# Kernel tuning notes

Hardware: AMD Instinct MI355X
Metric: run time of the kernel (lower is better)

Reference implementation:

```python
import jax, jax.numpy as jnp
import numpy as np

B, S, D, H, OUT = 256, 256, 512, 512, 128  # batch, time points, state dim (= hidden_size), MLP hidden, out_features


def setup_inputs() -> dict:
    key = jax.random.key(0)
    ks = jax.random.split(key, 6)
    # time channel: shared monotone grid (forward uses t[0] as the integration grid)
    t = jnp.linspace(0.0, 1.0, S)
    feats = jax.random.normal(ks[0], (B, S, D), dtype=jnp.float32) * 0.1
    x = jnp.concatenate([jnp.broadcast_to(t[None, :, None], (B, S, 1)), feats], axis=-1)  # [B,S,D+1]
    s1 = 1.0 / np.sqrt(D).astype(np.float32)
    s2 = 1.0 / np.sqrt(H).astype(np.float32)
    W1 = jax.random.normal(ks[1], (H, D), dtype=jnp.float32) * s1
    b1 = jnp.zeros((H,), dtype=jnp.float32)
    W2 = jax.random.normal(ks[2], (D, H), dtype=jnp.float32) * s2
    b2 = jnp.zeros((D,), dtype=jnp.float32)
    Wout = jax.random.normal(ks[3], (OUT, H), dtype=jnp.float32) * s2
    bout = jnp.zeros((OUT,), dtype=jnp.float32)
    return dict(x=x, W1=W1, b1=b1, W2=W2, b2=b2, Wout=Wout, bout=bout)


def reference(x, W1, b1, W2, b2, Wout, bout):
    t = x[0, :, 0]          # [S] integration grid (first sample's time channel)
    y0 = x[:, -1, 1:]       # [B, D] initial state

    def f(y):               # ODEFunc MLP: d -> h -> d
        return jnp.tanh(y @ W1.T + b1) @ W2.T + b2

    dts = t[1:] - t[:-1]    # [S-1]

    def rk4_step(y, dt):
        k1 = f(y)
        k2 = f(y + 0.5 * dt * k1)
        k3 = f(y + 0.5 * dt * k2)
        k4 = f(y + dt * k3)
        y_next = y + (dt / 6.0) * (k1 + 2.0 * k2 + 2.0 * k3 + k4)
        return y_next, None

    yT, _ = jax.lax.scan(rk4_step, y0, dts)  # solution[-1]: [B, D]
    return yT @ Wout.T + bout                # [B, OUT]
```

## Files before the change

kernel.cpp:

```cpp
#include <hip/hip_runtime.h>
#include <hip/hip_bf16.h>

typedef __attribute__((ext_vector_type(8))) short short8;
typedef __attribute__((ext_vector_type(8))) unsigned short ushort8;
typedef __attribute__((ext_vector_type(4))) float f32x4;
typedef __attribute__((ext_vector_type(4))) int int4v;
typedef __attribute__((ext_vector_type(4))) short short4v;

#define NB 256
#define NS 256
#define NH 512
#define NOUT 128
#define XROW 513

#define NCL 16
#define RPC 16
#define BPC 4
#define UBS 128
#define LPAD 520

#define OFF_DTS   0
#define OFF_Y0    4096
#define OFF_U0    (OFF_Y0 + NB*NH*4)
#define OFF_M     (OFF_U0 + NB*NH*4)
#define OFF_C     (OFF_M + NH*NH*2)
#define OFF_P     (OFF_C + 4096)
#define OFF_HG    (OFF_P + NOUT*NH*4)
#define OFF_HACC  (OFF_HG + NCL*2*RPC*NH*2)
#define OFF_FLAGS (OFF_HACC + NB*NH*4)

static __device__ __forceinline__ unsigned short bf16bits(float x) {
  return __builtin_bit_cast(unsigned short, __float2bfloat16(x));
}

static __device__ __forceinline__ void g_store8(void* addr, short4v v) {
  asm volatile("global_store_dwordx2 %0, %1, off sc0 sc1" :: "v"(addr), "v"(v) : "memory");
}
static __device__ __forceinline__ void g_store4(void* addr, unsigned v) {
  asm volatile("global_store_dword %0, %1, off sc0 sc1" :: "v"(addr), "v"(v) : "memory");
}
static __device__ __forceinline__ unsigned g_load4w(const void* addr) {
  unsigned v;
  asm volatile("global_load_dword %0, %1, off sc0 sc1\n\ts_waitcnt vmcnt(0)"
               : "=v"(v) : "v"(addr) : "memory");
  return v;
}
static __device__ __forceinline__ int4v g_load16(const void* addr) {
  int4v v;
  asm volatile("global_load_dwordx4 %0, %1, off sc0 sc1" : "=v"(v) : "v"(addr) : "memory");
  return v;
}
static __device__ __forceinline__ void wait_vm0() {
  asm volatile("s_waitcnt vmcnt(0)" ::: "memory");
}

static __device__ __forceinline__ float tanh_fast(float x) {
  x = fminf(fmaxf(x, -15.f), 15.f);
  float e = __expf(2.f * x);
  return (e - 1.f) * __builtin_amdgcn_rcpf(e + 1.f);
}


__global__ void k_dts(const float* __restrict__ x, float* __restrict__ dts) {
  int s = threadIdx.x;
  if (s < NS - 1) dts[s] = x[(s + 1) * XROW] - x[s * XROW];
  if (s == NS - 1) dts[NS - 1] = x[(NS - 1) * XROW] - x[0];
}

__global__ void k_y0(const float* __restrict__ x, float* __restrict__ y0) {
  int b = blockIdx.x;
  const float* src = x + (size_t)b * NS * XROW + (size_t)(NS - 1) * XROW + 1;
  for (int d = threadIdx.x; d < NH; d += blockDim.x) y0[b * NH + d] = src[d];
}

__global__ void k_c(const float* __restrict__ W1, const float* __restrict__ b2,
                    float* __restrict__ c) {
  int i = blockIdx.x * blockDim.x + threadIdx.x;
  if (i < NH) {
    float s = 0.f;
    for (int d = 0; d < NH; ++d) s += W1[i * NH + d] * b2[d];
    c[i] = s;
  }
}

__global__ void k_mm_nn_bf16(const float* __restrict__ A, const float* __restrict__ Bm,
                             __hip_bfloat16* __restrict__ C, int N, int K) {
  __shared__ float As[16][17], Bs[16][17];
  int tx = threadIdx.x & 15, ty = threadIdx.x >> 4;
  int m = blockIdx.y * 16 + ty, n = blockIdx.x * 16 + tx;
  float acc = 0.f;
  for (int k0 = 0; k0 < K; k0 += 16) {
    As[ty][tx] = A[m * K + k0 + tx];
    Bs[ty][tx] = Bm[(size_t)(k0 + ty) * N + n];
    __syncthreads();
#pragma unroll
    for (int kk = 0; kk < 16; ++kk) acc += As[ty][kk] * Bs[kk][tx];
    __syncthreads();
  }
  C[m * N + n] = __float2bfloat16(acc);
}

__global__ void k_mm_nn_f32(const float* __restrict__ A, const float* __restrict__ Bm,
                            float* __restrict__ C, int N, int K) {
  __shared__ float As[16][17], Bs[16][17];
  int tx = threadIdx.x & 15, ty = threadIdx.x >> 4;
  int m = blockIdx.y * 16 + ty, n = blockIdx.x * 16 + tx;
  float acc = 0.f;
  for (int k0 = 0; k0 < K; k0 += 16) {
    As[ty][tx] = A[m * K + k0 + tx];
    Bs[ty][tx] = Bm[(size_t)(k0 + ty) * N + n];
    __syncthreads();
#pragma unroll
    for (int kk = 0; kk < 16; ++kk) acc += As[ty][kk] * Bs[kk][tx];
    __syncthreads();
  }
  C[m * N + n] = acc;
}

__global__ void k_mm_nt_f32(const float* __restrict__ A, const float* __restrict__ Bm,
                            float* __restrict__ C, int N, int K) {
  __shared__ float As[16][17], Bs[16][17];
  int tx = threadIdx.x & 15, ty = threadIdx.x >> 4;
  int m = blockIdx.y * 16 + ty;
  int n0 = blockIdx.x * 16;
  float acc = 0.f;
  for (int k0 = 0; k0 < K; k0 += 16) {
    As[ty][tx] = A[m * K + k0 + tx];
    Bs[ty][tx] = Bm[(size_t)(n0 + ty) * K + k0 + tx];
    __syncthreads();
#pragma unroll
    for (int kk = 0; kk < 16; ++kk) acc += As[ty][kk] * Bs[tx][kk];
    __syncthreads();
  }
  C[m * N + n0 + tx] = acc;
}


__global__ __launch_bounds__(256) void k_main(
    const float* __restrict__ u0, const __hip_bfloat16* __restrict__ Mg,
    const float* __restrict__ cg, const float* __restrict__ b1g,
    const float* __restrict__ dtsg,
    __hip_bfloat16* __restrict__ hG, float* __restrict__ Hacc,
    unsigned int* __restrict__ flags)
{
  __shared__ __hip_bfloat16 Mlds[UBS][LPAD];
  __shared__ __hip_bfloat16 hlds[RPC][LPAD];
  __shared__ float dtl[NS];

  const int tid = threadIdx.x;
  const int bx = blockIdx.x;
  const int xcd = bx & 7, slot = bx >> 3;
  const int cl = xcd + ((slot >> 2) << 3);
  const int jb = slot & 3;
  const int lane = tid & 63, wv = tid >> 6;
  const int r = lane & 15, g4 = lane >> 4;
  const int row0 = cl * RPC;
  const int ub = jb * UBS;

  for (int i = tid; i < UBS * 64; i += 256) {
    int row = i >> 6, ch = (i & 63) * 8;
    *(ushort8*)&Mlds[row][ch] = *(const ushort8*)(Mg + (size_t)(ub + row) * NH + ch);
  }
  if (tid < NS) dtl[tid] = dtsg[tid];

  const int udl0 = wv * 32 + g4 * 4;
  float u[2][4], Wa[2][4], Hs[2][4], Ht[2][4], hr[2][4], wp[2][4];
  float b1r[2][4], cr[2][4];
#pragma unroll
  for (int t = 0; t < 2; ++t)
#pragma unroll
    for (int j = 0; j < 4; ++j) {
      int ud = ub + udl0 + t * 16 + j;
      u[t][j] = u0[(row0 + r) * NH + ud];
      b1r[t][j] = b1g[ud];
      cr[t][j] = cg[ud];
      Ht[t][j] = 0.f; wp[t][j] = 0.f; Wa[t][j] = 0.f; Hs[t][j] = 0.f;
    }
  __syncthreads();

  unsigned int* flg = flags + cl * 32;

  int sidx = 0;
  for (int step = 0; step < NS - 1; ++step) {
    float dt = dtl[step];
#pragma unroll 1
    for (int st = 0; st < 4; ++st, ++sidx) {
      float gam = (st == 0) ? 0.f : ((st == 3) ? dt : 0.5f * dt);
#pragma unroll
      for (int t = 0; t < 2; ++t)
#pragma unroll
        for (int j = 0; j < 4; ++j)
          hr[t][j] = tanh_fast(u[t][j] + gam * wp[t][j] + b1r[t][j]);

      int par = sidx & 1;
      __hip_bfloat16* hgp = hG + (size_t)(cl * 2 + par) * RPC * NH;
#pragma unroll
      for (int t = 0; t < 2; ++t) {
        short4v pk;
        pk.x = (short)bf16bits(hr[t][0]);
        pk.y = (short)bf16bits(hr[t][1]);
        pk.z = (short)bf16bits(hr[t][2]);
        pk.w = (short)bf16bits(hr[t][3]);
        int col = ub + udl0 + t * 16;
        g_store8(hgp + r * NH + col, pk);
        *(short4v*)&hlds[r][col] = pk;
      }
      wait_vm0();
      unsigned tgt = (unsigned)(sidx + 1);
      if (lane == 0) g_store4(flg + jb * 4 + wv, tgt);
      __syncthreads();

      f32x4 acc0 = {0.f, 0.f, 0.f, 0.f}, acc1 = {0.f, 0.f, 0.f, 0.f};
#pragma unroll
      for (int q = 0; q < 4; ++q) {
        int kc = ub + q * 32 + g4 * 8;
        short8 bf = *(const short8*)&hlds[r][kc];
        short8 a0 = *(const short8*)&Mlds[wv * 32 + r][kc];
        short8 a1 = *(const short8*)&Mlds[wv * 32 + 16 + r][kc];
        acc0 = __builtin_amdgcn_mfma_f32_16x16x32_bf16(a0, bf, acc0, 0, 0, 0);
        acc1 = __builtin_amdgcn_mfma_f32_16x16x32_bf16(a1, bf, acc1, 0, 0, 0);
      }

      {
        const unsigned int* fp = flg + (lane & 15);
        for (;;) {
          unsigned v = g_load4w(fp);
          if (__all((int)(v >= tgt))) break;
          __builtin_amdgcn_s_sleep(1);
        }
      }

      {
        int rr = tid >> 4, sl = tid & 15;
        int4v dv[3];
#pragma unroll
        for (int m = 0; m < 3; ++m) {
          int jr = (jb + 1 + m) & 3;
          dv[m] = g_load16(hgp + rr * NH + jr * UBS + sl * 8);
        }
        wait_vm0();
#pragma unroll
        for (int m = 0; m < 3; ++m) {
          int jr = (jb + 1 + m) & 3;
          *(int4v*)&hlds[rr][jr * UBS + sl * 8] = dv[m];
        }
      }
      __syncthreads();

#pragma unroll 1
      for (int m = 0; m < 3; ++m) {
        int jr = (jb + 1 + m) & 3;
#pragma unroll
        for (int q = 0; q < 4; ++q) {
          int kc = jr * UBS + q * 32 + g4 * 8;
          short8 bf = *(const short8*)&hlds[r][kc];
          short8 a0 = *(const short8*)&Mlds[wv * 32 + r][kc];
          short8 a1 = *(const short8*)&Mlds[wv * 32 + 16 + r][kc];
          acc0 = __builtin_amdgcn_mfma_f32_16x16x32_bf16(a0, bf, acc0, 0, 0, 0);
          acc1 = __builtin_amdgcn_mfma_f32_16x16x32_bf16(a1, bf, acc1, 0, 0, 0);
        }
      }

      float wc[2][4];
#pragma unroll
      for (int j = 0; j < 4; ++j) { wc[0][j] = acc0[j] + cr[0][j]; wc[1][j] = acc1[j] + cr[1][j]; }

      float cw = (st == 0 || st == 3) ? 1.f : 2.f;
#pragma unroll
      for (int t = 0; t < 2; ++t)
#pragma unroll
        for (int j = 0; j < 4; ++j) {
          if (st == 0) { Wa[t][j] = wc[t][j]; Hs[t][j] = hr[t][j]; }
          else { Wa[t][j] += cw * wc[t][j]; Hs[t][j] += cw * hr[t][j]; }
          wp[t][j] = wc[t][j];
        }
      if (st == 3) {
        float f6 = dt * (1.f / 6.f);
#pragma unroll
        for (int t = 0; t < 2; ++t)
#pragma unroll
          for (int j = 0; j < 4; ++j) {
            u[t][j] += f6 * Wa[t][j];
            Ht[t][j] += f6 * Hs[t][j];
          }
      }
    }
  }

#pragma unroll
  for (int t = 0; t < 2; ++t)
#pragma unroll
    for (int j = 0; j < 4; ++j)
      Hacc[(row0 + r) * NH + ub + udl0 + t * 16 + j] = Ht[t][j];
}

__global__ void k_epi(const float* __restrict__ y0, const float* __restrict__ Hacc,
                      const float* __restrict__ P, const float* __restrict__ Wout,
                      const float* __restrict__ b2, const float* __restrict__ bout,
                      const float* __restrict__ dtsg, float* __restrict__ out)
{
  __shared__ float ys[NH], hs[NH];
  int rr = blockIdx.x, o = threadIdx.x;
  float sdt = dtsg[NS - 1];
  for (int i = threadIdx.x; i < NH; i += blockDim.x) {
    ys[i] = y0[rr * NH + i] + sdt * b2[i];
    hs[i] = Hacc[rr * NH + i];
  }
  __syncthreads();
  float s = bout[o];
  const float* wr = Wout + o * NH;
  const float* pr = P + o * NH;
  for (int d = 0; d < NH; ++d) s += wr[d] * ys[d];
  for (int h = 0; h < NH; ++h) s += pr[h] * hs[h];
  out[rr * NOUT + o] = s;
}


extern "C" void kernel_launch(void* const* d_in, const int* in_sizes, int n_in,
                              void* d_out, int out_size, void* d_ws, size_t ws_size,
                              hipStream_t stream) {
  const float* x    = (const float*)d_in[0];
  const float* W1   = (const float*)d_in[1];
  const float* b1   = (const float*)d_in[2];
  const float* W2   = (const float*)d_in[3];
  const float* b2   = (const float*)d_in[4];
  const float* Wout = (const float*)d_in[5];
  const float* bout = (const float*)d_in[6];
  float* out = (float*)d_out;

  char* ws = (char*)d_ws;
  float*          dts  = (float*)(ws + OFF_DTS);
  float*          y0   = (float*)(ws + OFF_Y0);
  float*          u0   = (float*)(ws + OFF_U0);
  __hip_bfloat16* Mbf  = (__hip_bfloat16*)(ws + OFF_M);
  float*          cvec = (float*)(ws + OFF_C);
  float*          P    = (float*)(ws + OFF_P);
  __hip_bfloat16* hG   = (__hip_bfloat16*)(ws + OFF_HG);
  float*          Hac  = (float*)(ws + OFF_HACC);
  unsigned int*   flg  = (unsigned int*)(ws + OFF_FLAGS);

  hipMemsetAsync(flg, 0, NCL * 32 * 4, stream);

  k_dts<<<1, 256, 0, stream>>>(x, dts);
  k_y0 <<<NB, 256, 0, stream>>>(x, y0);
  k_c  <<<2, 256, 0, stream>>>(W1, b2, cvec);
  k_mm_nn_bf16<<<dim3(32, 32), 256, 0, stream>>>(W1, W2, Mbf, NH, NH);
  k_mm_nt_f32<<<dim3(32, 16), 256, 0, stream>>>(y0, W1, u0, NH, NH);
  k_mm_nn_f32<<<dim3(32, 8), 256, 0, stream>>>(Wout, W2, P, NH, NH);

  k_main<<<NCL * BPC, 256, 0, stream>>>(u0, Mbf, cvec, b1, dts, hG, Hac, flg);

  k_epi<<<NB, NOUT, 0, stream>>>(y0, Hac, P, Wout, b2, bout, dts, out);
}
```

Baseline: 2.696 ms.

## Replace flag-based cross-block sync with stamped data words in exchange buffer

Each bf16 hidden value is now packed into a 32-bit word together with a 16-bit step stamp, so consumers poll the data itself instead of waiting on separate flag writes. This removes the producer's store-wait-then-flag round trip and the separate flag-polling loop. The cost is double the exchange traffic, a block-wide barrier in every polling iteration, an extra barrier per stage, and a memset of the whole exchange buffer. Stamps wrap at 16 bits, which is fine for the 1020 stages here.

```diff
diff --git a/kernel.cpp b/kernel.cpp
--- a/kernel.cpp
+++ b/kernel.cpp
@@ -26,24 +26,15 @@
 #define OFF_C     (OFF_M + NH*NH*2)
 #define OFF_P     (OFF_C + 4096)
 #define OFF_HG    (OFF_P + NOUT*NH*4)
-#define OFF_HACC  (OFF_HG + NCL*2*RPC*NH*2)
-#define OFF_FLAGS (OFF_HACC + NB*NH*4)
-
-static __device__ __forceinline__ unsigned short bf16bits(float x) {
-  return __builtin_bit_cast(unsigned short, __float2bfloat16(x));
-}
-
-static __device__ __forceinline__ void g_store8(void* addr, short4v v) {
-  asm volatile("global_store_dwordx2 %0, %1, off sc0 sc1" :: "v"(addr), "v"(v) : "memory");
-}
-static __device__ __forceinline__ void g_store4(void* addr, unsigned v) {
-  asm volatile("global_store_dword %0, %1, off sc0 sc1" :: "v"(addr), "v"(v) : "memory");
-}
-static __device__ __forceinline__ unsigned g_load4w(const void* addr) {
-  unsigned v;
-  asm volatile("global_load_dword %0, %1, off sc0 sc1\n\ts_waitcnt vmcnt(0)"
-               : "=v"(v) : "v"(addr) : "memory");
-  return v;
+#define HG_BYTES  (NCL*2*RPC*NH*4)
+#define OFF_HACC  (OFF_HG + HG_BYTES)
+
+static __device__ __forceinline__ unsigned bf16bits(float x) {
+  return (unsigned)__builtin_bit_cast(unsigned short, __float2bfloat16(x));
+}
+
+static __device__ __forceinline__ void g_store16(void* addr, int4v v) {
+  asm volatile("global_store_dwordx4 %0, %1, off sc0 sc1" :: "v"(addr), "v"(v) : "memory");
 }
 static __device__ __forceinline__ int4v g_load16(const void* addr) {
   int4v v;
@@ -140,12 +131,12 @@
     const float* __restrict__ u0, const __hip_bfloat16* __restrict__ Mg,
     const float* __restrict__ cg, const float* __restrict__ b1g,
     const float* __restrict__ dtsg,
-    __hip_bfloat16* __restrict__ hG, float* __restrict__ Hacc,
-    unsigned int* __restrict__ flags)
+    float* __restrict__ hG, float* __restrict__ Hacc)
 {
   __shared__ __hip_bfloat16 Mlds[UBS][LPAD];
   __shared__ __hip_bfloat16 hlds[RPC][LPAD];
   __shared__ float dtl[NS];
+  __shared__ int okf[4];
 
   const int tid = threadIdx.x;
   const int bx = blockIdx.x;
@@ -156,6 +147,7 @@
   const int r = lane & 15, g4 = lane >> 4;
   const int row0 = cl * RPC;
   const int ub = jb * UBS;
+  const int rr = tid >> 4, sl = tid & 15;
 
   for (int i = tid; i < UBS * 64; i += 256) {
     int row = i >> 6, ch = (i & 63) * 8;
@@ -178,14 +170,13 @@
     }
   __syncthreads();
 
-  unsigned int* flg = flags + cl * 32;
-
   int sidx = 0;
   for (int step = 0; step < NS - 1; ++step) {
     float dt = dtl[step];
 #pragma unroll 1
     for (int st = 0; st < 4; ++st, ++sidx) {
       float gam = (st == 0) ? 0.f : ((st == 3) ? dt : 0.5f * dt);
+      unsigned stamp = (unsigned)(sidx + 1);
 #pragma unroll
       for (int t = 0; t < 2; ++t)
 #pragma unroll
@@ -193,21 +184,22 @@
           hr[t][j] = tanh_fast(u[t][j] + gam * wp[t][j] + b1r[t][j]);
 
       int par = sidx & 1;
-      __hip_bfloat16* hgp = hG + (size_t)(cl * 2 + par) * RPC * NH;
+      float* hgp = hG + (size_t)(cl * 2 + par) * RPC * NH;
 #pragma unroll
       for (int t = 0; t < 2; ++t) {
+        int col = ub + udl0 + t * 16;
+        unsigned hb0 = bf16bits(hr[t][0]), hb1 = bf16bits(hr[t][1]);
+        unsigned hb2 = bf16bits(hr[t][2]), hb3 = bf16bits(hr[t][3]);
+        int4v sv;
+        sv.x = (int)((hb0 << 16) | stamp);
+        sv.y = (int)((hb1 << 16) | stamp);
+        sv.z = (int)((hb2 << 16) | stamp);
+        sv.w = (int)((hb3 << 16) | stamp);
+        g_store16(hgp + r * NH + col, sv);
         short4v pk;
-        pk.x = (short)bf16bits(hr[t][0]);
-        pk.y = (short)bf16bits(hr[t][1]);
-        pk.z = (short)bf16bits(hr[t][2]);
-        pk.w = (short)bf16bits(hr[t][3]);
-        int col = ub + udl0 + t * 16;
-        g_store8(hgp + r * NH + col, pk);
+        pk.x = (short)hb0; pk.y = (short)hb1; pk.z = (short)hb2; pk.w = (short)hb3;
         *(short4v*)&hlds[r][col] = pk;
       }
-      wait_vm0();
-      unsigned tgt = (unsigned)(sidx + 1);
-      if (lane == 0) g_store4(flg + jb * 4 + wv, tgt);
       __syncthreads();
 
       f32x4 acc0 = {0.f, 0.f, 0.f, 0.f}, acc1 = {0.f, 0.f, 0.f, 0.f};
@@ -221,29 +213,40 @@
         acc1 = __builtin_amdgcn_mfma_f32_16x16x32_bf16(a1, bf, acc1, 0, 0, 0);
       }
 
-      {
-        const unsigned int* fp = flg + (lane & 15);
-        for (;;) {
-          unsigned v = g_load4w(fp);
-          if (__all((int)(v >= tgt))) break;
-          __builtin_amdgcn_s_sleep(1);
-        }
-      }
-
-      {
-        int rr = tid >> 4, sl = tid & 15;
-        int4v dv[3];
+      int4v dv[6];
+      for (;;) {
 #pragma unroll
         for (int m = 0; m < 3; ++m) {
           int jr = (jb + 1 + m) & 3;
-          dv[m] = g_load16(hgp + rr * NH + jr * UBS + sl * 8);
+          const float* base = hgp + rr * NH + jr * UBS + sl * 8;
+          dv[2 * m]     = g_load16(base);
+          dv[2 * m + 1] = g_load16(base + 4);
         }
         wait_vm0();
-#pragma unroll
-        for (int m = 0; m < 3; ++m) {
-          int jr = (jb + 1 + m) & 3;
-          *(int4v*)&hlds[rr][jr * UBS + sl * 8] = dv[m];
-        }
+        bool ok = true;
+#pragma unroll
+        for (int q = 0; q < 6; ++q)
+          ok &= (((unsigned)dv[q].x & 0xffffu) == stamp) &
+                (((unsigned)dv[q].y & 0xffffu) == stamp) &
+                (((unsigned)dv[q].z & 0xffffu) == stamp) &
+                (((unsigned)dv[q].w & 0xffffu) == stamp);
+        bool wok = __all((int)ok);
+        if (lane == 0) okf[wv] = wok ? 1 : 0;
+        __syncthreads();
+        if (okf[0] & okf[1] & okf[2] & okf[3]) break;
+        __syncthreads();
+        __builtin_amdgcn_s_sleep(1);
+      }
+#pragma unroll
+      for (int m = 0; m < 3; ++m) {
+        int jr = (jb + 1 + m) & 3;
+        int4v a = dv[2 * m], b = dv[2 * m + 1];
+        int4v pk;
+        pk.x = (int)(((unsigned)a.x >> 16) | ((unsigned)a.y & 0xffff0000u));
+        pk.y = (int)(((unsigned)a.z >> 16) | ((unsigned)a.w & 0xffff0000u));
+        pk.z = (int)(((unsigned)b.x >> 16) | ((unsigned)b.y & 0xffff0000u));
+        pk.w = (int)(((unsigned)b.z >> 16) | ((unsigned)b.w & 0xffff0000u));
+        *(int4v*)&hlds[rr][jr * UBS + sl * 8] = pk;
       }
       __syncthreads();
 
@@ -284,6 +287,7 @@
             Ht[t][j] += f6 * Hs[t][j];
           }
       }
+      __syncthreads();
     }
   }
 
@@ -335,11 +339,10 @@
   __hip_bfloat16* Mbf  = (__hip_bfloat16*)(ws + OFF_M);
   float*          cvec = (float*)(ws + OFF_C);
   float*          P    = (float*)(ws + OFF_P);
-  __hip_bfloat16* hG   = (__hip_bfloat16*)(ws + OFF_HG);
+  float*          hG   = (float*)(ws + OFF_HG);
   float*          Hac  = (float*)(ws + OFF_HACC);
-  unsigned int*   flg  = (unsigned int*)(ws + OFF_FLAGS);
-
-  hipMemsetAsync(flg, 0, NCL * 32 * 4, stream);
+
+  hipMemsetAsync(hG, 0, HG_BYTES, stream);
 
   k_dts<<<1, 256, 0, stream>>>(x, dts);
   k_y0 <<<NB, 256, 0, stream>>>(x, y0);
@@ -348,7 +351,7 @@
   k_mm_nt_f32<<<dim3(32, 16), 256, 0, stream>>>(y0, W1, u0, NH, NH);
   k_mm_nn_f32<<<dim3(32, 8), 256, 0, stream>>>(Wout, W2, P, NH, NH);
 
-  k_main<<<NCL * BPC, 256, 0, stream>>>(u0, Mbf, cvec, b1, dts, hG, Hac, flg);
+  k_main<<<NCL * BPC, 256, 0, stream>>>(u0, Mbf, cvec, b1, dts, hG, Hac);
 
   k_epi<<<NB, NOUT, 0, stream>>>(y0, Hac, P, Wout, b2, bout, dts, out);
 }
```

After: 3.638 ms. +34.9%, slower.

## Interleave two row groups per cluster to overlap cross-block exchange latency

Applied to the files above, without the earlier changes.

Each cluster of four blocks now handles two 16-row groups (A and B) instead of one, which halves the cluster count and the number of launched blocks. The two groups are software-pipelined within each RK stage. Group B's tanh and global publish run while group A waits on its flag poll and gather, and A's next-stage publish is issued before B's matmul finishes. The aim is to hide the inter-block flag and global-memory round trip behind useful work, at the cost of more registers, more barriers, and only 32 blocks on the GPU.

```diff
diff --git a/kernel.cpp b/kernel.cpp
--- a/kernel.cpp
+++ b/kernel.cpp
@@ -13,7 +13,7 @@
 #define NOUT 128
 #define XROW 513
 
-#define NCL 16
+#define NCL 8
 #define RPC 16
 #define BPC 4
 #define UBS 128
@@ -26,11 +26,12 @@
 #define OFF_C     (OFF_M + NH*NH*2)
 #define OFF_P     (OFF_C + 4096)
 #define OFF_HG    (OFF_P + NOUT*NH*4)
-#define OFF_HACC  (OFF_HG + NCL*2*RPC*NH*2)
+#define HG_BYTES  (NCL*2*2*RPC*NH*2)
+#define OFF_HACC  (OFF_HG + HG_BYTES)
 #define OFF_FLAGS (OFF_HACC + NB*NH*4)
 
-static __device__ __forceinline__ unsigned short bf16bits(float x) {
-  return __builtin_bit_cast(unsigned short, __float2bfloat16(x));
+static __device__ __forceinline__ unsigned bf16bits(float x) {
+  return (unsigned)__builtin_bit_cast(unsigned short, __float2bfloat16(x));
 }
 
 static __device__ __forceinline__ void g_store8(void* addr, short4v v) {
@@ -149,13 +150,12 @@
 
   const int tid = threadIdx.x;
   const int bx = blockIdx.x;
-  const int xcd = bx & 7, slot = bx >> 3;
-  const int cl = xcd + ((slot >> 2) << 3);
-  const int jb = slot & 3;
+  const int cl = bx & 7, jb = bx >> 3;
   const int lane = tid & 63, wv = tid >> 6;
   const int r = lane & 15, g4 = lane >> 4;
-  const int row0 = cl * RPC;
+  const int row0 = cl * 32;
   const int ub = jb * UBS;
+  const int rr = tid >> 4, sl = tid & 15;
 
   for (int i = tid; i < UBS * 64; i += 256) {
     int row = i >> 6, ch = (i & 63) * 8;
@@ -164,115 +164,136 @@
   if (tid < NS) dtl[tid] = dtsg[tid];
 
   const int udl0 = wv * 32 + g4 * 4;
-  float u[2][4], Wa[2][4], Hs[2][4], Ht[2][4], hr[2][4], wp[2][4];
+  float uA[2][4], WaA[2][4], HsA[2][4], HtA[2][4], hrA[2][4], wpA[2][4];
+  float uB[2][4], WaB[2][4], HsB[2][4], HtB[2][4], hrB[2][4], wpB[2][4];
   float b1r[2][4], cr[2][4];
 #pragma unroll
   for (int t = 0; t < 2; ++t)
 #pragma unroll
     for (int j = 0; j < 4; ++j) {
       int ud = ub + udl0 + t * 16 + j;
-      u[t][j] = u0[(row0 + r) * NH + ud];
       b1r[t][j] = b1g[ud];
       cr[t][j] = cg[ud];
-      Ht[t][j] = 0.f; wp[t][j] = 0.f; Wa[t][j] = 0.f; Hs[t][j] = 0.f;
-    }
-  __syncthreads();
-
-  unsigned int* flg = flags + cl * 32;
-
-  int sidx = 0;
-  for (int step = 0; step < NS - 1; ++step) {
+      uA[t][j] = u0[(row0 + r) * NH + ud];
+      uB[t][j] = u0[(row0 + 16 + r) * NH + ud];
+      HtA[t][j] = 0.f; wpA[t][j] = 0.f; WaA[t][j] = 0.f; HsA[t][j] = 0.f;
+      HtB[t][j] = 0.f; wpB[t][j] = 0.f; WaB[t][j] = 0.f; HsB[t][j] = 0.f;
+    }
+
+  unsigned int* flgA = flags + (cl * 2 + 0) * 32;
+  unsigned int* flgB = flags + (cl * 2 + 1) * 32;
+  auto hbuf = [&](int g, int par) {
+    return hG + (size_t)((cl * 2 + g) * 2 + par) * RPC * NH;
+  };
+
+  auto pub_g = [&](float hr[2][4], __hip_bfloat16* hgp, bool to_lds) {
+#pragma unroll
+    for (int t = 0; t < 2; ++t) {
+      int col = ub + udl0 + t * 16;
+      short4v pk;
+      pk.x = (short)bf16bits(hr[t][0]);
+      pk.y = (short)bf16bits(hr[t][1]);
+      pk.z = (short)bf16bits(hr[t][2]);
+      pk.w = (short)bf16bits(hr[t][3]);
+      g_store8(hgp + r * NH + col, pk);
+      if (to_lds) *(short4v*)&hlds[r][col] = pk;
+    }
+  };
+  auto poll = [&](unsigned int* flg, unsigned tgt) {
+    const unsigned int* fp = flg + (lane & 15);
+    for (;;) {
+      unsigned v = g_load4w(fp);
+      if (__all((int)(v >= tgt))) break;
+      __builtin_amdgcn_s_sleep(1);
+    }
+  };
+  auto gather = [&](__hip_bfloat16* hgp) {
+    int4v dv[3];
+#pragma unroll
+    for (int m = 0; m < 3; ++m) {
+      int jr = (jb + 1 + m) & 3;
+      dv[m] = g_load16(hgp + rr * NH + jr * UBS + sl * 8);
+    }
+    wait_vm0();
+#pragma unroll
+    for (int m = 0; m < 3; ++m) {
+      int jr = (jb + 1 + m) & 3;
+      *(int4v*)&hlds[rr][jr * UBS + sl * 8] = dv[m];
+    }
+  };
+
+#pragma unroll
+  for (int t = 0; t < 2; ++t)
+#pragma unroll
+    for (int j = 0; j < 4; ++j)
+      hrA[t][j] = tanh_fast(uA[t][j] + b1r[t][j]);
+  pub_g(hrA, hbuf(0, 0), true);
+
+#pragma unroll 1
+  for (int sidx = 0; sidx < 4 * (NS - 1); ++sidx) {
+    int st = sidx & 3, step = sidx >> 2;
     float dt = dtl[step];
+    float gam = (st == 0) ? 0.f : ((st == 3) ? dt : 0.5f * dt);
+    unsigned tgt = (unsigned)(sidx + 1);
+    int par = sidx & 1;
+    __hip_bfloat16* hgpA = hbuf(0, par);
+    __hip_bfloat16* hgpB = hbuf(1, par);
+
+    __syncthreads();
+
+    f32x4 a0A = {0.f, 0.f, 0.f, 0.f}, a1A = {0.f, 0.f, 0.f, 0.f};
+#pragma unroll
+    for (int q = 0; q < 4; ++q) {
+      int kc = ub + q * 32 + g4 * 8;
+      short8 bf = *(const short8*)&hlds[r][kc];
+      short8 m0 = *(const short8*)&Mlds[wv * 32 + r][kc];
+      short8 m1 = *(const short8*)&Mlds[wv * 32 + 16 + r][kc];
+      a0A = __builtin_amdgcn_mfma_f32_16x16x32_bf16(m0, bf, a0A, 0, 0, 0);
+      a1A = __builtin_amdgcn_mfma_f32_16x16x32_bf16(m1, bf, a1A, 0, 0, 0);
+    }
+
+#pragma unroll
+    for (int t = 0; t < 2; ++t)
+#pragma unroll
+      for (int j = 0; j < 4; ++j)
+        hrB[t][j] = tanh_fast(uB[t][j] + gam * wpB[t][j] + b1r[t][j]);
+    pub_g(hrB, hgpB, false);
+
+    wait_vm0();
+    if (lane == 0) {
+      g_store4(flgA + jb * 4 + wv, tgt);
+      g_store4(flgB + jb * 4 + wv, tgt);
+    }
+
+    poll(flgA, tgt);
+    gather(hgpA);
+    __syncthreads();
+
 #pragma unroll 1
-    for (int st = 0; st < 4; ++st, ++sidx) {
-      float gam = (st == 0) ? 0.f : ((st == 3) ? dt : 0.5f * dt);
+    for (int m = 0; m < 3; ++m) {
+      int jr = (jb + 1 + m) & 3;
+#pragma unroll
+      for (int q = 0; q < 4; ++q) {
+        int kc = jr * UBS + q * 32 + g4 * 8;
+        short8 bf = *(const short8*)&hlds[r][kc];
+        short8 m0 = *(const short8*)&Mlds[wv * 32 + r][kc];
+        short8 m1 = *(const short8*)&Mlds[wv * 32 + 16 + r][kc];
+        a0A = __builtin_amdgcn_mfma_f32_16x16x32_bf16(m0, bf, a0A, 0, 0, 0);
+        a1A = __builtin_amdgcn_mfma_f32_16x16x32_bf16(m1, bf, a1A, 0, 0, 0);
+      }
+    }
+    {
+      float wc[2][4];
+#pragma unroll
+      for (int j = 0; j < 4; ++j) { wc[0][j] = a0A[j] + cr[0][j]; wc[1][j] = a1A[j] + cr[1][j]; }
+      float cw = (st == 0 || st == 3) ? 1.f : 2.f;
 #pragma unroll
       for (int t = 0; t < 2; ++t)
 #pragma unroll
-        for (int j = 0; j < 4; ++j)
-          hr[t][j] = tanh_fast(u[t][j] + gam * wp[t][j] + b1r[t][j]);
-
-      int par = sidx & 1;
-      __hip_bfloat16* hgp = hG + (size_t)(cl * 2 + par) * RPC * NH;
-#pragma unroll
-      for (int t = 0; t < 2; ++t) {
-        short4v pk;
-        pk.x = (short)bf16bits(hr[t][0]);
-        pk.y = (short)bf16bits(hr[t][1]);
-        pk.z = (short)bf16bits(hr[t][2]);
-        pk.w = (short)bf16bits(hr[t][3]);
-        int col = ub + udl0 + t * 16;
-        g_store8(hgp + r * NH + col, pk);
-        *(short4v*)&hlds[r][col] = pk;
-      }
-      wait_vm0();
-      unsigned tgt = (unsigned)(sidx + 1);
-      if (lane == 0) g_store4(flg + jb * 4 + wv, tgt);
-      __syncthreads();
-
-      f32x4 acc0 = {0.f, 0.f, 0.f, 0.f}, acc1 = {0.f, 0.f, 0.f, 0.f};
-#pragma unroll
-      for (int q = 0; q < 4; ++q) {
-        int kc = ub + q * 32 + g4 * 8;
-        short8 bf = *(const short8*)&hlds[r][kc];
-        short8 a0 = *(const short8*)&Mlds[wv * 32 + r][kc];
-        short8 a1 = *(const short8*)&Mlds[wv * 32 + 16 + r][kc];
-        acc0 = __builtin_amdgcn_mfma_f32_16x16x32_bf16(a0, bf, acc0, 0, 0, 0);
-        acc1 = __builtin_amdgcn_mfma_f32_16x16x32_bf16(a1, bf, acc1, 0, 0, 0);
-      }
-
-      {
-        const unsigned int* fp = flg + (lane & 15);
-        for (;;) {
-          unsigned v = g_load4w(fp);
-          if (__all((int)(v >= tgt))) break;
-          __builtin_amdgcn_s_sleep(1);
-        }
-      }
-
-      {
-        int rr = tid >> 4, sl = tid & 15;
-        int4v dv[3];
-#pragma unroll
-        for (int m = 0; m < 3; ++m) {
-          int jr = (jb + 1 + m) & 3;
-          dv[m] = g_load16(hgp + rr * NH + jr * UBS + sl * 8);
-        }
-        wait_vm0();
-#pragma unroll
-        for (int m = 0; m < 3; ++m) {
-          int jr = (jb + 1 + m) & 3;
-          *(int4v*)&hlds[rr][jr * UBS + sl * 8] = dv[m];
-        }
-      }
-      __syncthreads();
-
-#pragma unroll 1
-      for (int m = 0; m < 3; ++m) {
-        int jr = (jb + 1 + m) & 3;
-#pragma unroll
-        for (int q = 0; q < 4; ++q) {
-          int kc = jr * UBS + q * 32 + g4 * 8;
-          short8 bf = *(const short8*)&hlds[r][kc];
-          short8 a0 = *(const short8*)&Mlds[wv * 32 + r][kc];
-          short8 a1 = *(const short8*)&Mlds[wv * 32 + 16 + r][kc];
-          acc0 = __builtin_amdgcn_mfma_f32_16x16x32_bf16(a0, bf, acc0, 0, 0, 0);
-          acc1 = __builtin_amdgcn_mfma_f32_16x16x32_bf16(a1, bf, acc1, 0, 0, 0);
-        }
-      }
-
-      float wc[2][4];
-#pragma unroll
-      for (int j = 0; j < 4; ++j) { wc[0][j] = acc0[j] + cr[0][j]; wc[1][j] = acc1[j] + cr[1][j]; }
-
-      float cw = (st == 0 || st == 3) ? 1.f : 2.f;
-#pragma unroll
-      for (int t = 0; t < 2; ++t)
-#pragma unroll
         for (int j = 0; j < 4; ++j) {
-          if (st == 0) { Wa[t][j] = wc[t][j]; Hs[t][j] = hr[t][j]; }
-          else { Wa[t][j] += cw * wc[t][j]; Hs[t][j] += cw * hr[t][j]; }
-          wp[t][j] = wc[t][j];
+          if (st == 0) { WaA[t][j] = wc[t][j]; HsA[t][j] = hrA[t][j]; }
+          else { WaA[t][j] += cw * wc[t][j]; HsA[t][j] += cw * hrA[t][j]; }
+          wpA[t][j] = wc[t][j];
         }
       if (st == 3) {
         float f6 = dt * (1.f / 6.f);
@@ -280,18 +301,88 @@
         for (int t = 0; t < 2; ++t)
 #pragma unroll
           for (int j = 0; j < 4; ++j) {
-            u[t][j] += f6 * Wa[t][j];
-            Ht[t][j] += f6 * Hs[t][j];
+            uA[t][j] += f6 * WaA[t][j];
+            HtA[t][j] += f6 * HsA[t][j];
           }
       }
     }
+    __syncthreads();
+
+#pragma unroll
+    for (int t = 0; t < 2; ++t) {
+      int col = ub + udl0 + t * 16;
+      short4v pk;
+      pk.x = (short)bf16bits(hrB[t][0]);
+      pk.y = (short)bf16bits(hrB[t][1]);
+      pk.z = (short)bf16bits(hrB[t][2]);
+      pk.w = (short)bf16bits(hrB[t][3]);
+      *(short4v*)&hlds[r][col] = pk;
+    }
+    poll(flgB, tgt);
+    gather(hgpB);
+    __syncthreads();
+
+    f32x4 a0B = {0.f, 0.f, 0.f, 0.f}, a1B = {0.f, 0.f, 0.f, 0.f};
+#pragma unroll 1
+    for (int m = 0; m < 4; ++m) {
+      int jr = (jb + m) & 3;
+#pragma unroll
+      for (int q = 0; q < 4; ++q) {
+        int kc = jr * UBS + q * 32 + g4 * 8;
+        short8 bf = *(const short8*)&hlds[r][kc];
+        short8 m0 = *(const short8*)&Mlds[wv * 32 + r][kc];
+        short8 m1 = *(const short8*)&Mlds[wv * 32 + 16 + r][kc];
+        a0B = __builtin_amdgcn_mfma_f32_16x16x32_bf16(m0, bf, a0B, 0, 0, 0);
+        a1B = __builtin_amdgcn_mfma_f32_16x16x32_bf16(m1, bf, a1B, 0, 0, 0);
+      }
+    }
+    {
+      float wc[2][4];
+#pragma unroll
+      for (int j = 0; j < 4; ++j) { wc[0][j] = a0B[j] + cr[0][j]; wc[1][j] = a1B[j] + cr[1][j]; }
+      float cw = (st == 0 || st == 3) ? 1.f : 2.f;
+#pragma unroll
+      for (int t = 0; t < 2; ++t)
+#pragma unroll
+        for (int j = 0; j < 4; ++j) {
+          if (st == 0) { WaB[t][j] = wc[t][j]; HsB[t][j] = hrB[t][j]; }
+          else { WaB[t][j] += cw * wc[t][j]; HsB[t][j] += cw * hrB[t][j]; }
+          wpB[t][j] = wc[t][j];
+        }
+      if (st == 3) {
+        float f6 = dt * (1.f / 6.f);
+#pragma unroll
+        for (int t = 0; t < 2; ++t)
+#pragma unroll
+          for (int j = 0; j < 4; ++j) {
+            uB[t][j] += f6 * WaB[t][j];
+            HtB[t][j] += f6 * HsB[t][j];
+          }
+      }
+    }
+    __syncthreads();
+
+    {
+      int nsidx = sidx + 1;
+      int nst = nsidx & 3, nstep = nsidx >> 2;
+      float gamn = (nst == 0) ? 0.f : ((nst == 3) ? dtl[nstep] : 0.5f * dtl[nstep]);
+#pragma unroll
+      for (int t = 0; t < 2; ++t)
+#pragma unroll
+        for (int j = 0; j < 4; ++j)
+          hrA[t][j] = tanh_fast(uA[t][j] + gamn * wpA[t][j] + b1r[t][j]);
+      pub_g(hrA, hbuf(0, nsidx & 1), true);
+    }
   }
 
 #pragma unroll
   for (int t = 0; t < 2; ++t)
 #pragma unroll
-    for (int j = 0; j < 4; ++j)
-      Hacc[(row0 + r) * NH + ub + udl0 + t * 16 + j] = Ht[t][j];
+    for (int j = 0; j < 4; ++j) {
+      int ud = ub + udl0 + t * 16 + j;
+      Hacc[(row0 + r) * NH + ud] = HtA[t][j];
+      Hacc[(row0 + 16 + r) * NH + ud] = HtB[t][j];
+    }
 }
 
 __global__ void k_epi(const float* __restrict__ y0, const float* __restrict__ Hacc,
@@ -339,7 +430,7 @@
   float*          Hac  = (float*)(ws + OFF_HACC);
   unsigned int*   flg  = (unsigned int*)(ws + OFF_FLAGS);
 
-  hipMemsetAsync(flg, 0, NCL * 32 * 4, stream);
+  hipMemsetAsync(flg, 0, NCL * 2 * 32 * 4, stream);
 
   k_dts<<<1, 256, 0, stream>>>(x, dts);
   k_y0 <<<NB, 256, 0, stream>>>(x, y0);
```

Result: slower. 6.174 ms (+129.0%).

## Overlap local MFMA with global store drain and load remote h directly into registers

Applied to the files above, without the earlier changes.

Moves the local-block MFMA ahead of the global store wait and flag publish, so compute overlaps the memory drain. Remote h tiles are loaded from global memory straight into registers in MFMA operand layout instead of being staged through LDS. This removes one __syncthreads and an LDS write/read round trip. It also drops the s_sleep from the spin loop and adds a trailing barrier to protect LDS reuse. The cost is higher register pressure (12 int4 vectors) and a busier spin loop.

```diff
diff --git a/kernel.cpp b/kernel.cpp
--- a/kernel.cpp
+++ b/kernel.cpp
@@ -26,11 +26,12 @@
 #define OFF_C     (OFF_M + NH*NH*2)
 #define OFF_P     (OFF_C + 4096)
 #define OFF_HG    (OFF_P + NOUT*NH*4)
-#define OFF_HACC  (OFF_HG + NCL*2*RPC*NH*2)
+#define HG_BYTES  (NCL*2*RPC*NH*2)
+#define OFF_HACC  (OFF_HG + HG_BYTES)
 #define OFF_FLAGS (OFF_HACC + NB*NH*4)
 
-static __device__ __forceinline__ unsigned short bf16bits(float x) {
-  return __builtin_bit_cast(unsigned short, __float2bfloat16(x));
+static __device__ __forceinline__ unsigned bf16bits(float x) {
+  return (unsigned)__builtin_bit_cast(unsigned short, __float2bfloat16(x));
 }
 
 static __device__ __forceinline__ void g_store8(void* addr, short4v v) {
@@ -52,6 +53,10 @@
 }
 static __device__ __forceinline__ void wait_vm0() {
   asm volatile("s_waitcnt vmcnt(0)" ::: "memory");
+}
+static __device__ __forceinline__ void bar_lgkm() {
+  asm volatile("s_waitcnt lgkmcnt(0)" ::: "memory");
+  __builtin_amdgcn_s_barrier();
 }
 
 static __device__ __forceinline__ float tanh_fast(float x) {
@@ -205,59 +210,55 @@
         g_store8(hgp + r * NH + col, pk);
         *(short4v*)&hlds[r][col] = pk;
       }
+      bar_lgkm();
+
+      f32x4 acc0 = {0.f, 0.f, 0.f, 0.f}, acc1 = {0.f, 0.f, 0.f, 0.f};
+#pragma unroll
+      for (int q = 0; q < 4; ++q) {
+        int kc = ub + q * 32 + g4 * 8;
+        short8 bf = *(const short8*)&hlds[r][kc];
+        short8 m0 = *(const short8*)&Mlds[wv * 32 + r][kc];
+        short8 m1 = *(const short8*)&Mlds[wv * 32 + 16 + r][kc];
+        acc0 = __builtin_amdgcn_mfma_f32_16x16x32_bf16(m0, bf, acc0, 0, 0, 0);
+        acc1 = __builtin_amdgcn_mfma_f32_16x16x32_bf16(m1, bf, acc1, 0, 0, 0);
+      }
+      __builtin_amdgcn_sched_barrier(0);
       wait_vm0();
       unsigned tgt = (unsigned)(sidx + 1);
       if (lane == 0) g_store4(flg + jb * 4 + wv, tgt);
-      __syncthreads();
-
-      f32x4 acc0 = {0.f, 0.f, 0.f, 0.f}, acc1 = {0.f, 0.f, 0.f, 0.f};
-#pragma unroll
-      for (int q = 0; q < 4; ++q) {
-        int kc = ub + q * 32 + g4 * 8;
-        short8 bf = *(const short8*)&hlds[r][kc];
-        short8 a0 = *(const short8*)&Mlds[wv * 32 + r][kc];
-        short8 a1 = *(const short8*)&Mlds[wv * 32 + 16 + r][kc];
-        acc0 = __builtin_amdgcn_mfma_f32_16x16x32_bf16(a0, bf, acc0, 0, 0, 0);
-        acc1 = __builtin_amdgcn_mfma_f32_16x16x32_bf16(a1, bf, acc1, 0, 0, 0);
-      }
 
       {
         const unsigned int* fp = flg + (lane & 15);
         for (;;) {
           unsigned v = g_load4w(fp);
           if (__all((int)(v >= tgt))) break;
-          __builtin_amdgcn_s_sleep(1);
         }
       }
 
+      int4v dv[12];
       {
-        int rr = tid >> 4, sl = tid & 15;
-        int4v dv[3];
+        const __hip_bfloat16* hb = hgp + r * NH;
 #pragma unroll
         for (int m = 0; m < 3; ++m) {
           int jr = (jb + 1 + m) & 3;
-          dv[m] = g_load16(hgp + rr * NH + jr * UBS + sl * 8);
+#pragma unroll
+          for (int q = 0; q < 4; ++q)
+            dv[m * 4 + q] = g_load16(hb + jr * UBS + q * 32 + g4 * 8);
         }
         wait_vm0();
-#pragma unroll
-        for (int m = 0; m < 3; ++m) {
-          int jr = (jb + 1 + m) & 3;
-          *(int4v*)&hlds[rr][jr * UBS + sl * 8] = dv[m];
-        }
-      }
-      __syncthreads();
-
-#pragma unroll 1
+        __builtin_amdgcn_sched_barrier(0);
+      }
+#pragma unroll
       for (int m = 0; m < 3; ++m) {
         int jr = (jb + 1 + m) & 3;
 #pragma unroll
         for (int q = 0; q < 4; ++q) {
           int kc = jr * UBS + q * 32 + g4 * 8;
-          short8 bf = *(const short8*)&hlds[r][kc];
-          short8 a0 = *(const short8*)&Mlds[wv * 32 + r][kc];
-          short8 a1 = *(const short8*)&Mlds[wv * 32 + 16 + r][kc];
-          acc0 = __builtin_amdgcn_mfma_f32_16x16x32_bf16(a0, bf, acc0, 0, 0, 0);
-          acc1 = __builtin_amdgcn_mfma_f32_16x16x32_bf16(a1, bf, acc1, 0, 0, 0);
+          short8 bf = __builtin_bit_cast(short8, dv[m * 4 + q]);
+          short8 m0 = *(const short8*)&Mlds[wv * 32 + r][kc];
+          short8 m1 = *(const short8*)&Mlds[wv * 32 + 16 + r][kc];
+          acc0 = __builtin_amdgcn_mfma_f32_16x16x32_bf16(m0, bf, acc0, 0, 0, 0);
+          acc1 = __builtin_amdgcn_mfma_f32_16x16x32_bf16(m1, bf, acc1, 0, 0, 0);
         }
       }
 
@@ -284,6 +285,7 @@
             Ht[t][j] += f6 * Hs[t][j];
           }
       }
+      bar_lgkm();
     }
   }
 
```

After: 4.846 ms. +79.7%, slower.
